# Performance work log

Hardware: AMD Instinct MI355X
Metric: run time of the kernel (lower is better)

The kernel has to match this reference:

```python
import jax, jax.numpy as jnp
import numpy as np

B, L, H, V = 256, 200, 128, 50000
NLAYER, K = 2, 20
NEG = -1e10


def setup_inputs() -> dict:
    key = jax.random.key(0)
    ks = jax.random.split(key, 14)
    lens = jax.random.randint(ks[0], (B,), 50, L + 1)
    pos = jnp.arange(L)
    valid = pos[None, :] < lens[:, None]                       # [B,L] bool
    seq = jnp.where(valid, jax.random.randint(ks[1], (B, L), 1, V), 0)
    lengths = valid.astype(jnp.int32)                          # >0 where real token
    reverse_lengths = jnp.where(valid, lens[:, None] - pos[None, :], 0)  # 1..len, 0=pad

    def nrm(k, shape, s=0.02):
        return jax.random.normal(k, shape, jnp.float32) * s

    emb_w = nrm(ks[2], (V, H)).at[0].set(0.0)
    wnoise_w = nrm(ks[3], (L + 1, H)).at[0].set(0.0)
    cluster_w = nrm(ks[4], (L + 1, 1)).at[0].set(0.0)
    ffn1_w = nrm(ks[5], (H, H), 0.05)
    ffn1_b = jnp.zeros((H,), jnp.float32)
    ffn2_w = nrm(ks[6], (H, H), 0.05)
    ffn2_b = jnp.zeros((H,), jnp.float32)
    ln_g = jnp.ones((H,), jnp.float32)
    ln_b = jnp.zeros((H,), jnp.float32)
    gate_w = nrm(ks[7], (2 * H, H), 0.05)
    coff = jax.random.normal(ks[8], (NLAYER, B, L, L), jnp.float32)  # fixed noise (torch.normal)
    return dict(seq=seq, lengths=lengths, reverse_lengths=reverse_lengths,
                emb_w=emb_w, wnoise_w=wnoise_w, cluster_w=cluster_w,
                ffn1_w=ffn1_w, ffn1_b=ffn1_b, ffn2_w=ffn2_w, ffn2_b=ffn2_b,
                ln_g=ln_g, ln_b=ln_b, gate_w=gate_w, coff=coff)


def _sp(x):  # torch.nn.Softplus(threshold=1): identity above 1
    return jnp.where(x > 1.0, x, jnp.log1p(jnp.exp(jnp.minimum(x, 1.0))))


def _forward(seq, lengths, reverse_lengths, emb_w, wnoise_w, cluster_w,
             ffn1_w, ffn1_b, ffn2_w, ffn2_b, ln_g, ln_b, gate_w, coff):
    b, l = seq.shape
    mask = (lengths > 0).astype(jnp.float32)                   # [B,L]
    hidden = emb_w[seq]                                        # [B,L,H]
    slen = jnp.sum(mask, axis=1)                               # [B]
    e_s = hidden[jnp.arange(b), (slen - 1).astype(jnp.int32)]  # last real token state
    zero_layer = jnp.sum(hidden, 1) / slen[:, None]
    layer_collect = [zero_layer]
    eye = jnp.eye(l, dtype=hidden.dtype)
    pair_ok = mask[:, :, None] * mask[:, None, :]              # [B,L,L]
    for i in range(coff.shape[0]):
        wn = wnoise_w[reverse_lengths]                         # [B,L,H]
        sim = jnp.einsum('bld,bmd->blm', hidden, hidden)
        nrm = jnp.linalg.norm(hidden, axis=2, keepdims=True)   # [B,L,1]
        sim = sim / (nrm * nrm.transpose(0, 2, 1) + 1e-6)      # cosine similarity
        diag = cluster_w[reverse_lengths][..., 0]              # [B,L]
        sim = sim + diag[:, :, None] * eye                     # diag_embed add
        sim = sim + coff[i] * _sp(jnp.einsum('bld,bmd->blm', hidden, wn))
        msim = jnp.where(pair_ok == 0.0, NEG, sim)             # masked_fill
        _, idx = jax.lax.top_k(msim, K)                        # [B,L,K]
        sel = jnp.zeros_like(msim).at[jnp.arange(b)[:, None, None],
                                      jnp.arange(l)[None, :, None], idx].set(1.0)
        edges = sel * (msim > NEG).astype(msim.dtype)          # top-k & above-threshold
        cluster_label = edges.transpose(0, 2, 1)
        sim_softmax = jax.nn.softmax(msim, axis=2)
        ssm = cluster_label * sim_softmax                      # [B,L,L] sparse-weighted
        update_hidden = jnp.einsum('blm,bmd->bld', ssm, hidden)
        cmask = jnp.sum(ssm, axis=2)                           # [B,L]
        cmask = cmask / jnp.maximum(jnp.linalg.norm(cmask, axis=1, keepdims=True), 1e-12)
        if i > 0:
            update_hidden = update_hidden * (slen > 1.0).astype(hidden.dtype)[:, None, None]
        feed1 = jax.nn.relu(update_hidden @ ffn1_w + ffn1_b)
        pre = feed1 @ ffn2_w + ffn2_b + update_hidden          # dropout = identity (eval)
        mu = jnp.mean(pre, -1, keepdims=True)
        var = jnp.var(pre, -1, keepdims=True)
        feed2 = (pre - mu) / jnp.sqrt(var + 1e-5) * ln_g + ln_b
        layer_collect.append(jnp.sum(feed2 * cmask[:, :, None], 1))
    e_c = jnp.mean(jnp.stack(layer_collect, 1), 1)             # [B,H]
    alpha = jax.nn.sigmoid(jnp.concatenate([e_c, e_s], -1) @ gate_w)
    sess = alpha * e_c + (1.0 - alpha) * e_s
    scores = sess @ emb_w.T                                    # [B,V]
    return scores


def reference(seq, lengths, reverse_lengths, emb_w, wnoise_w, cluster_w,
              ffn1_w, ffn1_b, ffn2_w, ffn2_b, ln_g, ln_b, gate_w, coff):
    scores = _forward(seq, lengths, reverse_lengths, emb_w, wnoise_w, cluster_w,
                      ffn1_w, ffn1_b, ffn2_w, ffn2_b, ln_g, ln_b, gate_w, coff)
    return (scores, jnp.asarray(0.0, jnp.float32))  # con_loss == 0 when abs=True
```

## Files before the change

### kernel.cpp

```cpp
#include <hip/hip_runtime.h>
#include <cstdint>
#include <cstddef>

namespace {
constexpr int B = 256, L = 200, H = 128, V = 50000, TK = 20;
constexpr int NT = 1563;
constexpr float NEGV = -1e10f;
}

using bf16x8 = __attribute__((ext_vector_type(8))) short;
using s16x8  = __attribute__((ext_vector_type(8))) short;
using f32x16 = __attribute__((ext_vector_type(16))) float;

__device__ inline unsigned short f2bf(float f) {
  unsigned int u = __float_as_uint(f);
  unsigned int r = (u + 0x7fffu + ((u >> 16) & 1u)) >> 16;
  return (unsigned short)r;
}

#define DPP_QUAD_XOR1 0xB1
#define DPP_QUAD_XOR2 0x4E
#define DPP_ROW_HMIRR 0x141
#define DPP_ROW_MIRR  0x140

template <int CTRL>
__device__ inline unsigned dpp16_max_step(unsigned v) {
  unsigned t = (unsigned)__builtin_amdgcn_update_dpp(0, (int)v, CTRL, 0xF, 0xF, true);
  return v > t ? v : t;
}
__device__ inline unsigned grp16_max(unsigned v) {
  v = dpp16_max_step<DPP_QUAD_XOR1>(v);
  v = dpp16_max_step<DPP_QUAD_XOR2>(v);
  v = dpp16_max_step<DPP_ROW_HMIRR>(v);
  v = dpp16_max_step<DPP_ROW_MIRR>(v);
  return v;
}
template <int CTRL>
__device__ inline float dpp16_add_step(float v) {
  int t = __builtin_amdgcn_update_dpp(0, __float_as_int(v), CTRL, 0xF, 0xF, true);
  return v + __int_as_float(t);
}
__device__ inline float grp16_sum(float v) {
  v = dpp16_add_step<DPP_QUAD_XOR1>(v);
  v = dpp16_add_step<DPP_QUAD_XOR2>(v);
  v = dpp16_add_step<DPP_ROW_HMIRR>(v);
  v = dpp16_add_step<DPP_ROW_MIRR>(v);
  return v;
}

__device__ inline unsigned f2key(float f) {
  unsigned b = __float_as_uint(f);
  unsigned m = (unsigned)((int)b >> 31);
  return b ^ (m | 0x80000000u);
}
__device__ inline float key2f(unsigned u) {
  unsigned b = (u & 0x80000000u) ? (u & 0x7fffffffu) : ~u;
  return __uint_as_float(b);
}

__global__ __launch_bounds__(256) void k_embed(const int* __restrict__ seq,
                                               const int* __restrict__ rev,
                                               const float* __restrict__ emb,
                                               const float* __restrict__ wnoise,
                                               float* __restrict__ hidden,
                                               float* __restrict__ nrm,
                                               s16x8* __restrict__ hbh,
                                               s16x8* __restrict__ hbl,
                                               s16x8* __restrict__ wnh,
                                               s16x8* __restrict__ wnl) {
  int b = blockIdx.x / 7, lt = blockIdx.x % 7;
  int t = threadIdx.x;
  int r = t >> 3, c2 = t & 7;
  int l = lt * 32 + r;
  bool valid = l < L;
  float vv[16], wv[16];
  if (valid) {
    int row = b * L + l;
    int tok = seq[row];
    const float4* ep = (const float4*)&emb[(size_t)tok * H + c2 * 16];
    const float4* wp = (const float4*)&wnoise[(size_t)rev[row] * H + c2 * 16];
#pragma unroll
    for (int i = 0; i < 4; ++i) {
      float4 x = ep[i];
      vv[i * 4 + 0] = x.x; vv[i * 4 + 1] = x.y; vv[i * 4 + 2] = x.z; vv[i * 4 + 3] = x.w;
      float4 y = wp[i];
      wv[i * 4 + 0] = y.x; wv[i * 4 + 1] = y.y; wv[i * 4 + 2] = y.z; wv[i * 4 + 3] = y.w;
    }
  } else {
#pragma unroll
    for (int i = 0; i < 16; ++i) { vv[i] = 0.f; wv[i] = 0.f; }
  }
  if (valid) {
    int row = b * L + l;
#pragma unroll
    for (int i = 0; i < 4; ++i)
      *(float4*)&hidden[(size_t)row * H + c2 * 16 + i * 4] =
          make_float4(vv[i * 4], vv[i * 4 + 1], vv[i * 4 + 2], vv[i * 4 + 3]);
    float s = 0.f;
#pragma unroll
    for (int i = 0; i < 16; ++i) s += vv[i] * vv[i];
    s += __shfl_down(s, 4, 8);
    s += __shfl_down(s, 2, 8);
    s += __shfl_down(s, 1, 8);
    if (c2 == 0) nrm[row] = sqrtf(s);
  }
  s16x8 h0, h1, l0, l1, w0, w1, x0, x1;
#pragma unroll
  for (int i = 0; i < 8; ++i) {
    unsigned short hi = f2bf(vv[i]);
    h0[i] = (short)hi;
    l0[i] = (short)f2bf(vv[i] - __uint_as_float((unsigned)hi << 16));
    unsigned short wh = f2bf(wv[i]);
    w0[i] = (short)wh;
    x0[i] = (short)f2bf(wv[i] - __uint_as_float((unsigned)wh << 16));
  }
#pragma unroll
  for (int i = 0; i < 8; ++i) {
    unsigned short hi = f2bf(vv[8 + i]);
    h1[i] = (short)hi;
    l1[i] = (short)f2bf(vv[8 + i] - __uint_as_float((unsigned)hi << 16));
    unsigned short wh = f2bf(wv[8 + i]);
    w1[i] = (short)wh;
    x1[i] = (short)f2bf(wv[8 + i] - __uint_as_float((unsigned)wh << 16));
  }
  size_t fi0 = ((size_t)(b * 7 + lt) * 8 + c2) * 64 + r;
  size_t fi1 = fi0 + 32;
  hbh[fi0] = h0; hbh[fi1] = h1;
  hbl[fi0] = l0; hbl[fi1] = l1;
  wnh[fi0] = w0; wnh[fi1] = w1;
  wnl[fi0] = x0; wnl[fi1] = x1;
}

__global__ __launch_bounds__(512) void k_init(const int* __restrict__ lengths,
                                              const float* __restrict__ hidden,
                                              float* __restrict__ ecacc,
                                              float* __restrict__ e_s) {
  int b = blockIdx.x, tid = threadIdx.x;
  __shared__ float part[4][128];
  __shared__ int wcnt[8];
  __shared__ int s_slen;
  int c = (tid < L && lengths[b * L + tid] > 0) ? 1 : 0;
  for (int o = 32; o > 0; o >>= 1) c += __shfl_down(c, o, 64);
  if ((tid & 63) == 0) wcnt[tid >> 6] = c;
  __syncthreads();
  if (tid == 0) {
    int s = 0;
#pragma unroll
    for (int i = 0; i < 8; ++i) s += wcnt[i];
    s_slen = s;
  }
  int h = tid & 127, seg = tid >> 7;
  float s = 0.f;
  for (int l = seg; l < L; l += 4) s += hidden[(size_t)(b * L + l) * H + h];
  part[seg][h] = s;
  __syncthreads();
  if (tid < 128) {
    float tot = part[0][h] + part[1][h] + part[2][h] + part[3][h];
    int slen = s_slen;
    ecacc[b * H + h] = tot / (float)slen;
    e_s[b * H + h] = hidden[(size_t)(b * L + slen - 1) * H + h];
  }
}

__global__ __launch_bounds__(256) void k_simws(const s16x8* __restrict__ hbh,
                                               const s16x8* __restrict__ hbl,
                                               const s16x8* __restrict__ wnh,
                                               const s16x8* __restrict__ wnl,
                                               const float* __restrict__ nrm,
                                               const int* __restrict__ rev,
                                               const float* __restrict__ cluster,
                                               float* __restrict__ S0,
                                               float* __restrict__ WS) {
  int orig = blockIdx.x;
  int xcd = orig & 7, slot = orig >> 3;
  int b = xcd * 32 + slot / 14;
  int rem = slot % 14;
  int lt = rem >> 1, half = rem & 1;
  int wid = threadIdx.x >> 6, lane = threadIdx.x & 63;
  int mt = half * 4 + wid;
  if (mt > 6) return;
  int lr = lane & 31, kh = lane >> 5;
  size_t abase = ((size_t)(b * 7 + lt) * 8) * 64 + lane;
  bf16x8 ah[8], al[8];
#pragma unroll
  for (int ks = 0; ks < 8; ++ks) {
    ah[ks] = (bf16x8)hbh[abase + ks * 64];
    al[ks] = (bf16x8)hbl[abase + ks * 64];
  }
  size_t bbase = ((size_t)(b * 7 + mt) * 8) * 64 + lane;
  f32x16 accs = {}, accw = {};
#pragma unroll
  for (int ks = 0; ks < 8; ++ks) {
    bf16x8 bhh = (bf16x8)hbh[bbase + ks * 64];
    bf16x8 bhl = (bf16x8)hbl[bbase + ks * 64];
    bf16x8 bwh = (bf16x8)wnh[bbase + ks * 64];
    bf16x8 bwl = (bf16x8)wnl[bbase + ks * 64];
    accs = __builtin_amdgcn_mfma_f32_32x32x16_bf16(ah[ks], bhh, accs, 0, 0, 0);
    accs = __builtin_amdgcn_mfma_f32_32x32x16_bf16(ah[ks], bhl, accs, 0, 0, 0);
    accs = __builtin_amdgcn_mfma_f32_32x32x16_bf16(al[ks], bhh, accs, 0, 0, 0);
    accw = __builtin_amdgcn_mfma_f32_32x32x16_bf16(ah[ks], bwh, accw, 0, 0, 0);
    accw = __builtin_amdgcn_mfma_f32_32x32x16_bf16(ah[ks], bwl, accw, 0, 0, 0);
    accw = __builtin_amdgcn_mfma_f32_32x32x16_bf16(al[ks], bwh, accw, 0, 0, 0);
  }
  int m = mt * 32 + lr;
  if (m < L) {
    float nm = nrm[b * L + m];
#pragma unroll
    for (int r = 0; r < 16; ++r) {
      int row = lt * 32 + (r & 3) + 8 * (r >> 2) + 4 * kh;
      if (row < L) {
        float nl = nrm[b * L + row];
        float s0 = accs[r] * __builtin_amdgcn_rcpf(nl * nm + 1e-6f);
        if (row == m) s0 += cluster[rev[b * L + row]];
        size_t o = (size_t)(b * L + row) * L + m;
        S0[o] = s0;
        float x = accw[r];
        WS[o] = (x > 1.f) ? x : __logf(1.f + __expf(x));
      }
    }
  }
}

__global__ __launch_bounds__(256) void k_rowpass(const float* __restrict__ S0,
                                                 const float* __restrict__ WS,
                                                 const float* __restrict__ coff_i,
                                                 const int* __restrict__ lengths,
                                                 float* __restrict__ P,
                                                 unsigned char* __restrict__ ET) {
  __shared__ unsigned klds[256 * 27];
  int wid = threadIdx.x >> 6, lane = threadIdx.x & 63;
  int g = lane >> 4, q = lane & 15;
  int bb = blockIdx.x / 7, blk = blockIdx.x % 7;
  int g16 = wid * 4 + g;
  int lA = blk * 32 + g16 * 2, lB = lA + 1;
  bool lvA = lA < L, lvB = lB < L;
  int lrowA = bb * L + (lvA ? lA : 0);
  int lrowB = bb * L + (lvB ? lB : 0);
  bool mA = lvA && (lengths[lrowA] > 0);
  bool mB = lvB && (lengths[lrowB] > 0);
  size_t baseA = (size_t)lrowA * L, baseB = (size_t)lrowB * L;
  int kbA = threadIdx.x * 27, kbB = kbA + 13;
  float valA[13], valB[13]; unsigned vmA = 0, vmB = 0;
  unsigned a0 = 0, a1 = 0, a2 = 0; int aj0 = 0, aj1 = 0, aj2 = 0;
  unsigned c0 = 0, c1 = 0, c2 = 0; int cj0 = 0, cj1 = 0, cj2 = 0;
#pragma unroll
  for (int j = 0; j < 13; ++j) {
    int m = q + 16 * j;
    bool colOk = (m < L) && (lengths[bb * L + m] > 0);
    bool okA = mA && colOk, okB = mB && colOk;
    float vA = 0.f, vB = 0.f;
    if (okA) vA = S0[baseA + m] + coff_i[baseA + m] * WS[baseA + m];
    if (okB) vB = S0[baseB + m] + coff_i[baseB + m] * WS[baseB + m];
    valA[j] = vA; valB[j] = vB;
    unsigned kA = okA ? f2key(vA) : 0u;
    unsigned kB = okB ? f2key(vB) : 0u;
    vmA |= okA ? (1u << j) : 0u;
    vmB |= okB ? (1u << j) : 0u;
    klds[kbA + j] = kA;
    klds[kbB + j] = kB;
    if (kA > a0)      { a2 = a1; aj2 = aj1; a1 = a0; aj1 = aj0; a0 = kA; aj0 = j; }
    else if (kA > a1) { a2 = a1; aj2 = aj1; a1 = kA; aj1 = j; }
    else if (kA > a2) { a2 = kA; aj2 = j; }
    if (kB > c0)      { c2 = c1; cj2 = cj1; c1 = c0; cj1 = cj0; c0 = kB; cj0 = j; }
    else if (kB > c1) { c2 = c1; cj2 = cj1; c1 = kB; cj1 = j; }
    else if (kB > c2) { c2 = kB; cj2 = j; }
  }
  unsigned ccA = a0; int cjA = aj0; int consA = 0;
  unsigned ccB = c0; int cjB = cj0; int consB = 0;
  unsigned MuA = 0u, MuB = 0u;
  for (int t = 0; t < TK; ++t) {
    unsigned gmA = grp16_max(ccA);
    unsigned gmB = grp16_max(ccB);
    if (t == 0) { MuA = gmA; MuB = gmB; }
    if (__all((gmA | gmB) == 0u)) break;
    unsigned long long balA = __ballot(ccA == gmA && gmA != 0u);
    unsigned long long balB = __ballot(ccB == gmB && gmB != 0u);
    unsigned long long grpm = 0xFFFFull << (g * 16);
    unsigned long long mineA = balA & grpm;
    unsigned long long mineB = balB & grpm;
    int ownA = mineA ? (int)__builtin_ctzll(mineA) : -1;
    int ownB = mineB ? (int)__builtin_ctzll(mineB) : -1;
    if (lane == ownA) {
      int m = q + 16 * cjA;
      ET[((size_t)bb * L + m) * L + lA] = 1;
      klds[kbA + cjA] = 0u;
      ++consA;
      if (consA == 1)      { ccA = a1; cjA = aj1; }
      else if (consA == 2) { ccA = a2; cjA = aj2; }
      else {
        unsigned x = 0; int xj = 0;
#pragma unroll
        for (int j = 0; j < 13; ++j) {
          unsigned k2 = klds[kbA + j];
          if (k2 > x) { x = k2; xj = j; }
        }
        ccA = x; cjA = xj;
      }
    }
    if (lane == ownB) {
      int m = q + 16 * cjB;
      ET[((size_t)bb * L + m) * L + lB] = 1;
      klds[kbB + cjB] = 0u;
      ++consB;
      if (consB == 1)      { ccB = c1; cjB = cj1; }
      else if (consB == 2) { ccB = c2; cjB = cj2; }
      else {
        unsigned x = 0; int xj = 0;
#pragma unroll
        for (int j = 0; j < 13; ++j) {
          unsigned k2 = klds[kbB + j];
          if (k2 > x) { x = k2; xj = j; }
        }
        ccB = x; cjB = xj;
      }
    }
  }
  float MA = key2f(MuA), MB = key2f(MuB);
  float eA[13], eB[13]; float sA = 0.f, sB = 0.f;
#pragma unroll
  for (int j = 0; j < 13; ++j) {
    float evA = ((vmA >> j) & 1u) ? __expf(valA[j] - MA) : 0.f;
    float evB = ((vmB >> j) & 1u) ? __expf(valB[j] - MB) : 0.f;
    eA[j] = evA; sA += evA;
    eB[j] = evB; sB += evB;
  }
  sA = grp16_sum(sA);
  sB = grp16_sum(sB);
  float invA = (sA > 0.f) ? __builtin_amdgcn_rcpf(sA) : 0.f;
  float invB = (sB > 0.f) ? __builtin_amdgcn_rcpf(sB) : 0.f;
#pragma unroll
  for (int j = 0; j < 13; ++j) {
    int m = q + 16 * j;
    if (m < L) {
      if (lvA) P[baseA + m] = eA[j] * invA;
      if (lvB) P[baseB + m] = eB[j] * invB;
    }
  }
}

__global__ __launch_bounds__(512) void k_gather(const float* __restrict__ P,
                                                const unsigned char* __restrict__ ET,
                                                const float* __restrict__ hidden,
                                                float* __restrict__ cmask,
                                                float* __restrict__ upd) {
  __shared__ float wls[4][224];
  __shared__ unsigned char ils[4][224];
  __shared__ int s_cnt[4];
  int wv = threadIdx.x >> 6, lane = threadIdx.x & 63;
  if (wv < 4) {
    int rowW = blockIdx.x * 4 + wv;
    size_t baseW = (size_t)rowW * L;
    float w[4]; float s = 0.f;
#pragma unroll
    for (int j = 0; j < 4; ++j) {
      int m = lane + 64 * j;
      float ww = 0.f;
      if (m < L) ww = P[baseW + m] * (float)ET[baseW + m];
      w[j] = ww; s += ww;
    }
    float ssum = s;
    for (int off = 1; off < 64; off <<= 1) ssum += __shfl_xor(ssum, off, 64);
    if (lane == 0) cmask[rowW] = ssum;
    int pos_base = 0;
#pragma unroll
    for (int j = 0; j < 4; ++j) {
      bool nz = (w[j] != 0.f);
      unsigned long long mk = __ballot(nz);
      int rank = __popcll(mk & ((1ull << lane) - 1ull));
      if (nz) {
        int pos = pos_base + rank;
        ils[wv][pos] = (unsigned char)(lane + 64 * j);
        wls[wv][pos] = w[j];
      }
      pos_base += (int)__popcll(mk);
    }
    if (lane == 0) s_cnt[wv] = pos_base;
    int padEnd = ((pos_base + TK - 1) / TK) * TK;
    for (int p = pos_base + lane; p < padEnd; p += 64) {
      ils[wv][p] = 0; wls[wv][p] = 0.f;
    }
  }
  __syncthreads();
  int half = threadIdx.x >> 7;
  int h = threadIdx.x & 127;
  int row = blockIdx.x * 4 + half;
  int b = row / L;
  int n = s_cnt[half];
  float acc = 0.f;
  for (int e0 = 0; e0 < n; e0 += TK) {
    float w[TK]; int m[TK];
#pragma unroll
    for (int e = 0; e < TK; ++e) { w[e] = wls[half][e0 + e]; m[e] = ils[half][e0 + e]; }
    float hv[TK];
#pragma unroll
    for (int e = 0; e < TK; ++e)
      hv[e] = hidden[(size_t)(b * L + m[e]) * H + h];
#pragma unroll
    for (int e = 0; e < TK; ++e)
      acc += w[e] * hv[e];
  }
  upd[(size_t)row * H + h] = acc;
}

__global__ __launch_bounds__(64) void k_cnorm(float* __restrict__ cmask) {
  int b = blockIdx.x, lane = threadIdx.x;
  float v[4]; float s = 0.f;
#pragma unroll
  for (int j = 0; j < 4; ++j) {
    int l = lane + 64 * j;
    float x = (l < L) ? cmask[b * L + l] : 0.f;
    v[j] = x; s += x * x;
  }
  for (int off = 1; off < 64; off <<= 1) s += __shfl_xor(s, off, 64);
  float inv = 1.f / fmaxf(sqrtf(s), 1e-12f);
#pragma unroll
  for (int j = 0; j < 4; ++j) {
    int l = lane + 64 * j;
    if (l < L) cmask[b * L + l] = v[j] * inv;
  }
}

__global__ __launch_bounds__(256) void k_ffn(float* __restrict__ upd,
                                             const float* __restrict__ W1,
                                             const float* __restrict__ b1,
                                             const float* __restrict__ W2,
                                             const float* __restrict__ b2,
                                             const float* __restrict__ g,
                                             const float* __restrict__ beta,
                                             const float* __restrict__ cmask) {
  constexpr int AS = 136;
  __shared__ __align__(16) char smem[4 * 64 * AS * 2];
  short* ahs = (short*)smem;
  short* als = ahs + 64 * AS;
  short* f1h = (short*)(smem + 2 * 64 * AS * 2);
  short* f1l = f1h + 64 * AS;
  float (*ps)[132] = (float (*)[132])smem;
  __shared__ float mus[64], rsd[64];
  int row0 = blockIdx.x * 64;
  int tid = threadIdx.x;
  int wid = tid >> 6, lane = tid & 63;
  int lr = lane & 31, kh = lane >> 5;
  int n0 = wid * 32;
  int n = n0 + lr;
#pragma unroll
  for (int it = 0; it < 8; ++it) {
    int f = it * 256 + tid;
    int r = f >> 5, c4 = (f & 31) * 4;
    float4 v = *(const float4*)&upd[(size_t)(row0 + r) * H + c4];
    float vv[4] = {v.x, v.y, v.z, v.w};
    unsigned short hh[4]; short ll[4];
#pragma unroll
    for (int q2 = 0; q2 < 4; ++q2) {
      hh[q2] = f2bf(vv[q2]);
      ll[q2] = (short)f2bf(vv[q2] - __uint_as_float((unsigned)hh[q2] << 16));
    }
    uint2 ph = make_uint2((unsigned)hh[0] | ((unsigned)hh[1] << 16),
                          (unsigned)hh[2] | ((unsigned)hh[3] << 16));
    uint2 pl = make_uint2((unsigned short)ll[0] | ((unsigned)(unsigned short)ll[1] << 16),
                          (unsigned short)ll[2] | ((unsigned)(unsigned short)ll[3] << 16));
    *(uint2*)&ahs[r * AS + c4] = ph;
    *(uint2*)&als[r * AS + c4] = pl;
  }
  __syncthreads();
  bf16x8 wfh[8], wfl[8];
#pragma unroll
  for (int ks = 0; ks < 8; ++ks) {
#pragma unroll
    for (int i = 0; i < 8; ++i) {
      float w = W1[(size_t)(ks * 16 + kh * 8 + i) * H + n];
      unsigned short hi = f2bf(w);
      wfh[ks][i] = (short)hi;
      wfl[ks][i] = (short)f2bf(w - __uint_as_float((unsigned)hi << 16));
    }
  }
  f32x16 acc0, acc1;
  {
    float bv = b1[n];
#pragma unroll
    for (int r = 0; r < 16; ++r) { acc0[r] = bv; acc1[r] = bv; }
  }
#pragma unroll
  for (int ks = 0; ks < 8; ++ks) {
    bf16x8 xh0 = *(const bf16x8*)&ahs[(0 * 32 + lr) * AS + ks * 16 + kh * 8];
    bf16x8 xl0 = *(const bf16x8*)&als[(0 * 32 + lr) * AS + ks * 16 + kh * 8];
    bf16x8 xh1 = *(const bf16x8*)&ahs[(1 * 32 + lr) * AS + ks * 16 + kh * 8];
    bf16x8 xl1 = *(const bf16x8*)&als[(1 * 32 + lr) * AS + ks * 16 + kh * 8];
    acc0 = __builtin_amdgcn_mfma_f32_32x32x16_bf16(xh0, wfh[ks], acc0, 0, 0, 0);
    acc0 = __builtin_amdgcn_mfma_f32_32x32x16_bf16(xl0, wfh[ks], acc0, 0, 0, 0);
    acc0 = __builtin_amdgcn_mfma_f32_32x32x16_bf16(xh0, wfl[ks], acc0, 0, 0, 0);
    acc1 = __builtin_amdgcn_mfma_f32_32x32x16_bf16(xh1, wfh[ks], acc1, 0, 0, 0);
    acc1 = __builtin_amdgcn_mfma_f32_32x32x16_bf16(xl1, wfh[ks], acc1, 0, 0, 0);
    acc1 = __builtin_amdgcn_mfma_f32_32x32x16_bf16(xh1, wfl[ks], acc1, 0, 0, 0);
  }
#pragma unroll
  for (int r = 0; r < 16; ++r) {
    int crow = (r & 3) + 8 * (r >> 2) + 4 * kh;
    float f0 = fmaxf(acc0[r], 0.f);
    unsigned short h0 = f2bf(f0);
    f1h[crow * AS + n] = (short)h0;
    f1l[crow * AS + n] = (short)f2bf(f0 - __uint_as_float((unsigned)h0 << 16));
    float f1v = fmaxf(acc1[r], 0.f);
    unsigned short h1 = f2bf(f1v);
    f1h[(32 + crow) * AS + n] = (short)h1;
    f1l[(32 + crow) * AS + n] = (short)f2bf(f1v - __uint_as_float((unsigned)h1 << 16));
  }
  __syncthreads();
#pragma unroll
  for (int ks = 0; ks < 8; ++ks) {
#pragma unroll
    for (int i = 0; i < 8; ++i) {
      float w = W2[(size_t)(ks * 16 + kh * 8 + i) * H + n];
      unsigned short hi = f2bf(w);
      wfh[ks][i] = (short)hi;
      wfl[ks][i] = (short)f2bf(w - __uint_as_float((unsigned)hi << 16));
    }
  }
  {
    float bv = b2[n];
#pragma unroll
    for (int r = 0; r < 16; ++r) { acc0[r] = bv; acc1[r] = bv; }
  }
#pragma unroll
  for (int ks = 0; ks < 8; ++ks) {
    bf16x8 xh0 = *(const bf16x8*)&f1h[(0 * 32 + lr) * AS + ks * 16 + kh * 8];
    bf16x8 xl0 = *(const bf16x8*)&f1l[(0 * 32 + lr) * AS + ks * 16 + kh * 8];
    bf16x8 xh1 = *(const bf16x8*)&f1h[(1 * 32 + lr) * AS + ks * 16 + kh * 8];
    bf16x8 xl1 = *(const bf16x8*)&f1l[(1 * 32 + lr) * AS + ks * 16 + kh * 8];
    acc0 = __builtin_amdgcn_mfma_f32_32x32x16_bf16(xh0, wfh[ks], acc0, 0, 0, 0);
    acc0 = __builtin_amdgcn_mfma_f32_32x32x16_bf16(xl0, wfh[ks], acc0, 0, 0, 0);
    acc0 = __builtin_amdgcn_mfma_f32_32x32x16_bf16(xh0, wfl[ks], acc0, 0, 0, 0);
    acc1 = __builtin_amdgcn_mfma_f32_32x32x16_bf16(xh1, wfh[ks], acc1, 0, 0, 0);
    acc1 = __builtin_amdgcn_mfma_f32_32x32x16_bf16(xl1, wfh[ks], acc1, 0, 0, 0);
    acc1 = __builtin_amdgcn_mfma_f32_32x32x16_bf16(xh1, wfl[ks], acc1, 0, 0, 0);
  }
#pragma unroll
  for (int r = 0; r < 16; ++r) {
    int crow = (r & 3) + 8 * (r >> 2) + 4 * kh;
    float p0 = acc0[r] + upd[(size_t)(row0 + crow) * H + n];
    float p1 = acc1[r] + upd[(size_t)(row0 + 32 + crow) * H + n];
    acc0[r] = p0; acc1[r] = p1;
    ps[crow][n] = p0;
    ps[32 + crow][n] = p1;
  }
  __syncthreads();
  {
    int r = tid >> 2, sub = tid & 3;
    float s = 0.f, sq = 0.f;
#pragma unroll
    for (int j = 0; j < 8; ++j) {
      float4 x = *(const float4*)&ps[r][sub * 32 + j * 4];
      s += x.x + x.y + x.z + x.w;
      sq += x.x * x.x + x.y * x.y + x.z * x.z + x.w * x.w;
    }
    s += __shfl_down(s, 2, 4);  s += __shfl_down(s, 1, 4);
    sq += __shfl_down(sq, 2, 4); sq += __shfl_down(sq, 1, 4);
    if (sub == 0) {
      float mu = s * (1.f / 128.f);
      float var = sq * (1.f / 128.f) - mu * mu;
      mus[r] = mu;
      rsd[r] = rsqrtf(var + 1e-5f);
    }
  }
  __syncthreads();
  {
    float gn = g[n], bn = beta[n];
#pragma unroll
    for (int r = 0; r < 16; ++r) {
      int crow = (r & 3) + 8 * (r >> 2) + 4 * kh;
      float o0 = ((acc0[r] - mus[crow]) * rsd[crow] * gn + bn) * cmask[row0 + crow];
      float o1 = ((acc1[r] - mus[32 + crow]) * rsd[32 + crow] * gn + bn) * cmask[row0 + 32 + crow];
      upd[(size_t)(row0 + crow) * H + n] = o0;
      upd[(size_t)(row0 + 32 + crow) * H + n] = o1;
    }
  }
}

__global__ __launch_bounds__(512) void k_ecadd(const float* __restrict__ wf,
                                               float* __restrict__ ecacc) {
  int b = blockIdx.x, tid = threadIdx.x;
  __shared__ float part[4][128];
  int h = tid & 127, seg = tid >> 7;
  float s = 0.f;
  for (int l = seg; l < L; l += 4) s += wf[(size_t)(b * L + l) * H + h];
  part[seg][h] = s;
  __syncthreads();
  if (tid < 128)
    ecacc[b * H + h] += part[0][h] + part[1][h] + part[2][h] + part[3][h];
}

__global__ __launch_bounds__(256) void k_embconv(const float* __restrict__ emb,
                                                 s16x8* __restrict__ ebh,
                                                 s16x8* __restrict__ ebl) {
  int nt = blockIdx.x;
  int t = threadIdx.x;
  int r = t >> 3, c2 = t & 7;
  int n = nt * 32 + r;
  float vv[16];
  if (n < V) {
    const float4* ep = (const float4*)&emb[(size_t)n * H + c2 * 16];
#pragma unroll
    for (int i = 0; i < 4; ++i) {
      float4 x = ep[i];
      vv[i * 4 + 0] = x.x; vv[i * 4 + 1] = x.y; vv[i * 4 + 2] = x.z; vv[i * 4 + 3] = x.w;
    }
  } else {
#pragma unroll
    for (int i = 0; i < 16; ++i) vv[i] = 0.f;
  }
  s16x8 h0, h1, l0, l1;
#pragma unroll
  for (int i = 0; i < 8; ++i) {
    unsigned short hi = f2bf(vv[i]);
    h0[i] = (short)hi;
    l0[i] = (short)f2bf(vv[i] - __uint_as_float((unsigned)hi << 16));
    unsigned short hj = f2bf(vv[8 + i]);
    h1[i] = (short)hj;
    l1[i] = (short)f2bf(vv[8 + i] - __uint_as_float((unsigned)hj << 16));
  }
  size_t fi0 = ((size_t)nt * 8 + c2) * 64 + r;
  size_t fi1 = fi0 + 32;
  ebh[fi0] = h0; ebh[fi1] = h1;
  ebl[fi0] = l0; ebl[fi1] = l1;
}

__global__ __launch_bounds__(128) void k_gate(const float* __restrict__ ecacc,
                                              const float* __restrict__ e_s,
                                              const float* __restrict__ gw,
                                              float* __restrict__ sess,
                                              float* __restrict__ out) {
  __shared__ float cat[256];
  int b = blockIdx.x, h = threadIdx.x;
  float ec = ecacc[b * H + h] * (1.f / 3.f);
  float es = e_s[b * H + h];
  cat[h] = ec; cat[128 + h] = es;
  __syncthreads();
  float a = 0.f;
  for (int j = 0; j < 256; ++j) a = fmaf(cat[j], gw[(size_t)j * H + h], a);
  a = 1.f / (1.f + __expf(-a));
  sess[b * H + h] = a * ec + (1.f - a) * es;
  if (b == 0 && h == 0) out[(size_t)B * V] = 0.f;
}

__global__ __launch_bounds__(256) void k_scores(const float* __restrict__ sess,
                                                const s16x8* __restrict__ ebh,
                                                const s16x8* __restrict__ ebl,
                                                float* __restrict__ out) {
  int wid = threadIdx.x >> 6, lane = threadIdx.x & 63;
  int lr = lane & 31, kh = lane >> 5;
  int mt = blockIdx.y;
  int m = mt * 32 + lr;
  bf16x8 ah[8], al[8];
#pragma unroll
  for (int ks = 0; ks < 8; ++ks) {
    const float* sp = &sess[(size_t)m * H + ks * 16 + kh * 8];
    float4 a = *(const float4*)sp;
    float4 c = *(const float4*)(sp + 4);
    float av[8] = {a.x, a.y, a.z, a.w, c.x, c.y, c.z, c.w};
#pragma unroll
    for (int i = 0; i < 8; ++i) {
      unsigned short hi = f2bf(av[i]);
      ah[ks][i] = (short)hi;
      al[ks][i] = (short)f2bf(av[i] - __uint_as_float((unsigned)hi << 16));
    }
  }
  int ntEnd = min(blockIdx.x * 16 + 16, NT);
  for (int nt = blockIdx.x * 16 + wid; nt < ntEnd; nt += 4) {
    size_t bbase = ((size_t)nt * 8) * 64 + lane;
    f32x16 acc = {};
#pragma unroll
    for (int ks = 0; ks < 8; ++ks) {
      bf16x8 bh = (bf16x8)ebh[bbase + ks * 64];
      bf16x8 bl = (bf16x8)ebl[bbase + ks * 64];
      acc = __builtin_amdgcn_mfma_f32_32x32x16_bf16(ah[ks], bh, acc, 0, 0, 0);
      acc = __builtin_amdgcn_mfma_f32_32x32x16_bf16(al[ks], bh, acc, 0, 0, 0);
      acc = __builtin_amdgcn_mfma_f32_32x32x16_bf16(ah[ks], bl, acc, 0, 0, 0);
    }
    int n = nt * 32 + lr;
    if (n < V) {
#pragma unroll
      for (int r = 0; r < 16; ++r) {
        int row = mt * 32 + (r & 3) + 8 * (r >> 2) + 4 * kh;
        out[(size_t)row * V + n] = acc[r];
      }
    }
  }
}

extern "C" void kernel_launch(void* const* d_in, const int* in_sizes, int n_in,
                              void* d_out, int out_size, void* d_ws, size_t ws_size,
                              hipStream_t stream) {
  const int*   seq  = (const int*)d_in[0];
  const int*   lens = (const int*)d_in[1];
  const int*   rev  = (const int*)d_in[2];
  const float* emb  = (const float*)d_in[3];
  const float* wnz  = (const float*)d_in[4];
  const float* clw  = (const float*)d_in[5];
  const float* w1   = (const float*)d_in[6];
  const float* fb1  = (const float*)d_in[7];
  const float* w2   = (const float*)d_in[8];
  const float* fb2  = (const float*)d_in[9];
  const float* lng  = (const float*)d_in[10];
  const float* lnb  = (const float*)d_in[11];
  const float* gw   = (const float*)d_in[12];
  const float* coff = (const float*)d_in[13];
  float* out = (float*)d_out;

  char* ws = (char*)d_ws;
  size_t off = 0;
  auto alloc = [&](size_t bytes) {
    void* p = ws + off;
    off += (bytes + 255) & ~(size_t)255;
    return p;
  };
  float* hidden = (float*)alloc((size_t)B * L * H * 4);
  float* nrm    = (float*)alloc((size_t)B * L * 4);
  float* S0     = (float*)alloc((size_t)B * L * L * 4);
  float* WS     = (float*)alloc((size_t)B * L * L * 4);
  float* P      = (float*)alloc((size_t)B * L * L * 4);
  float* upd    = (float*)alloc((size_t)B * L * H * 4);
  float* cmask  = (float*)alloc((size_t)B * L * 4);
  int*   cnt    = (int*)alloc((size_t)B * L * 4);
  float* e_s    = (float*)alloc((size_t)B * H * 4);
  float* ecacc  = (float*)alloc((size_t)B * H * 4);
  float* sess   = (float*)alloc((size_t)B * H * 4);
  unsigned char* ET = (unsigned char*)alloc((size_t)B * L * L);
  s16x8* hbh = (s16x8*)alloc((size_t)B * 7 * 8 * 64 * 16);
  s16x8* wnh = (s16x8*)alloc((size_t)B * 7 * 8 * 64 * 16);
  s16x8* hbl = (s16x8*)P;
  s16x8* wnl = (s16x8*)upd;
  s16x8* ebh = (s16x8*)S0;
  s16x8* ebl = (s16x8*)WS;

  k_embed<<<B * 7, 256, 0, stream>>>(seq, rev, emb, wnz, hidden, nrm,
                                     hbh, hbl, wnh, wnl);
  k_init<<<B, 512, 0, stream>>>(lens, hidden, ecacc, e_s);
  k_simws<<<B * 14, 256, 0, stream>>>(hbh, hbl, wnh, wnl, nrm, rev, clw, S0, WS);

  for (int i = 0; i < 2; ++i) {
    hipMemsetAsync(ET, 0, (size_t)B * L * L, stream);
    k_rowpass<<<B * 7, 256, 0, stream>>>(S0, WS, coff + (size_t)i * B * L * L,
                                         lens, P, ET);
    k_gather<<<B * L / 4, 512, 0, stream>>>(P, ET, hidden, cmask, upd);
    k_cnorm<<<B, 64, 0, stream>>>(cmask);
    k_ffn<<<B * L / 64, 256, 0, stream>>>(upd, w1, fb1, w2, fb2, lng, lnb, cmask);
    k_ecadd<<<B, 512, 0, stream>>>(upd, ecacc);
  }

  k_embconv<<<NT, 256, 0, stream>>>(emb, ebh, ebl);
  k_gate<<<B, 128, 0, stream>>>(ecacc, e_s, gw, sess, out);
  k_scores<<<dim3((NT + 15) / 16, 8), 256, 0, stream>>>(sess, ebh, ebl, out);
}
```

Measured before the change: 463.4 us.

## Compute both layers' row-pass in one kernel sharing S0/WS loads

The per-layer row-pass kernel is replaced by a single kernel that handles both layers, because S0 and WS do not depend on the layer. Each row's S0/WS values are read once and combined with both layers' noise tensors, producing two probability matrices and two top-k edge masks. The LDS key buffer is dropped in favour of a consumed-bitmask that recomputes keys from registers. The cost is an extra full P buffer and ET buffer, plus higher register pressure from holding two layers' state per thread.

```diff
diff --git a/kernel.cpp b/kernel.cpp
--- a/kernel.cpp
+++ b/kernel.cpp
@@ -221,52 +221,52 @@
   }
 }
 
-__global__ __launch_bounds__(256) void k_rowpass(const float* __restrict__ S0,
-                                                 const float* __restrict__ WS,
-                                                 const float* __restrict__ coff_i,
-                                                 const int* __restrict__ lengths,
-                                                 float* __restrict__ P,
-                                                 unsigned char* __restrict__ ET) {
-  __shared__ unsigned klds[256 * 27];
+__global__ __launch_bounds__(256) void k_rowpass2(const float* __restrict__ S0,
+                                                  const float* __restrict__ WS,
+                                                  const float* __restrict__ coff,
+                                                  const int* __restrict__ lengths,
+                                                  float* __restrict__ P1,
+                                                  float* __restrict__ P2,
+                                                  unsigned char* __restrict__ ET1,
+                                                  unsigned char* __restrict__ ET2) {
   int wid = threadIdx.x >> 6, lane = threadIdx.x & 63;
   int g = lane >> 4, q = lane & 15;
-  int bb = blockIdx.x / 7, blk = blockIdx.x % 7;
-  int g16 = wid * 4 + g;
-  int lA = blk * 32 + g16 * 2, lB = lA + 1;
-  bool lvA = lA < L, lvB = lB < L;
-  int lrowA = bb * L + (lvA ? lA : 0);
-  int lrowB = bb * L + (lvB ? lB : 0);
-  bool mA = lvA && (lengths[lrowA] > 0);
-  bool mB = lvB && (lengths[lrowB] > 0);
-  size_t baseA = (size_t)lrowA * L, baseB = (size_t)lrowB * L;
-  int kbA = threadIdx.x * 27, kbB = kbA + 13;
-  float valA[13], valB[13]; unsigned vmA = 0, vmB = 0;
+  int bb = blockIdx.x / 13, blk = blockIdx.x % 13;
+  int l = blk * 16 + wid * 4 + g;
+  bool lvalid = l < L;
+  int lrow = bb * L + (lvalid ? l : 0);
+  bool mask_l = lvalid && (lengths[lrow] > 0);
+  size_t base = (size_t)lrow * L;
+  const float* c0 = coff;
+  const float* c1 = coff + (size_t)B * L * L;
+  float valA[13], valB[13]; unsigned okm = 0;
   unsigned a0 = 0, a1 = 0, a2 = 0; int aj0 = 0, aj1 = 0, aj2 = 0;
-  unsigned c0 = 0, c1 = 0, c2 = 0; int cj0 = 0, cj1 = 0, cj2 = 0;
+  unsigned b0 = 0, b1 = 0, b2 = 0; int bj0 = 0, bj1 = 0, bj2 = 0;
 #pragma unroll
   for (int j = 0; j < 13; ++j) {
     int m = q + 16 * j;
-    bool colOk = (m < L) && (lengths[bb * L + m] > 0);
-    bool okA = mA && colOk, okB = mB && colOk;
-    float vA = 0.f, vB = 0.f;
-    if (okA) vA = S0[baseA + m] + coff_i[baseA + m] * WS[baseA + m];
-    if (okB) vB = S0[baseB + m] + coff_i[baseB + m] * WS[baseB + m];
+    bool ok = false; float vA = 0.f, vB = 0.f;
+    if (mask_l && m < L) {
+      ok = lengths[bb * L + m] > 0;
+      if (ok) {
+        float a = S0[base + m], w = WS[base + m];
+        vA = a + c0[base + m] * w;
+        vB = a + c1[base + m] * w;
+      }
+    }
     valA[j] = vA; valB[j] = vB;
-    unsigned kA = okA ? f2key(vA) : 0u;
-    unsigned kB = okB ? f2key(vB) : 0u;
-    vmA |= okA ? (1u << j) : 0u;
-    vmB |= okB ? (1u << j) : 0u;
-    klds[kbA + j] = kA;
-    klds[kbB + j] = kB;
+    okm |= ok ? (1u << j) : 0u;
+    unsigned kA = ok ? f2key(vA) : 0u;
+    unsigned kB = ok ? f2key(vB) : 0u;
     if (kA > a0)      { a2 = a1; aj2 = aj1; a1 = a0; aj1 = aj0; a0 = kA; aj0 = j; }
     else if (kA > a1) { a2 = a1; aj2 = aj1; a1 = kA; aj1 = j; }
     else if (kA > a2) { a2 = kA; aj2 = j; }
-    if (kB > c0)      { c2 = c1; cj2 = cj1; c1 = c0; cj1 = cj0; c0 = kB; cj0 = j; }
-    else if (kB > c1) { c2 = c1; cj2 = cj1; c1 = kB; cj1 = j; }
-    else if (kB > c2) { c2 = kB; cj2 = j; }
-  }
-  unsigned ccA = a0; int cjA = aj0; int consA = 0;
-  unsigned ccB = c0; int cjB = cj0; int consB = 0;
+    if (kB > b0)      { b2 = b1; bj2 = bj1; b1 = b0; bj1 = bj0; b0 = kB; bj0 = j; }
+    else if (kB > b1) { b2 = b1; bj2 = bj1; b1 = kB; bj1 = j; }
+    else if (kB > b2) { b2 = kB; bj2 = j; }
+  }
+  unsigned ccA = a0; int cjA = aj0; int consA = 0; unsigned cmA = 0;
+  unsigned ccB = b0; int cjB = bj0; int consB = 0; unsigned cmB = 0;
   unsigned MuA = 0u, MuB = 0u;
   for (int t = 0; t < TK; ++t) {
     unsigned gmA = grp16_max(ccA);
@@ -282,8 +282,8 @@
     int ownB = mineB ? (int)__builtin_ctzll(mineB) : -1;
     if (lane == ownA) {
       int m = q + 16 * cjA;
-      ET[((size_t)bb * L + m) * L + lA] = 1;
-      klds[kbA + cjA] = 0u;
+      ET1[((size_t)bb * L + m) * L + l] = 1;
+      cmA |= 1u << cjA;
       ++consA;
       if (consA == 1)      { ccA = a1; cjA = aj1; }
       else if (consA == 2) { ccA = a2; cjA = aj2; }
@@ -291,7 +291,8 @@
         unsigned x = 0; int xj = 0;
 #pragma unroll
         for (int j = 0; j < 13; ++j) {
-          unsigned k2 = klds[kbA + j];
+          bool avail = ((okm >> j) & 1u) && !((cmA >> j) & 1u);
+          unsigned k2 = avail ? f2key(valA[j]) : 0u;
           if (k2 > x) { x = k2; xj = j; }
         }
         ccA = x; cjA = xj;
@@ -299,16 +300,17 @@
     }
     if (lane == ownB) {
       int m = q + 16 * cjB;
-      ET[((size_t)bb * L + m) * L + lB] = 1;
-      klds[kbB + cjB] = 0u;
+      ET2[((size_t)bb * L + m) * L + l] = 1;
+      cmB |= 1u << cjB;
       ++consB;
-      if (consB == 1)      { ccB = c1; cjB = cj1; }
-      else if (consB == 2) { ccB = c2; cjB = cj2; }
+      if (consB == 1)      { ccB = b1; cjB = bj1; }
+      else if (consB == 2) { ccB = b2; cjB = bj2; }
       else {
         unsigned x = 0; int xj = 0;
 #pragma unroll
         for (int j = 0; j < 13; ++j) {
-          unsigned k2 = klds[kbB + j];
+          bool avail = ((okm >> j) & 1u) && !((cmB >> j) & 1u);
+          unsigned k2 = avail ? f2key(valB[j]) : 0u;
           if (k2 > x) { x = k2; xj = j; }
         }
         ccB = x; cjB = xj;
@@ -319,8 +321,9 @@
   float eA[13], eB[13]; float sA = 0.f, sB = 0.f;
 #pragma unroll
   for (int j = 0; j < 13; ++j) {
-    float evA = ((vmA >> j) & 1u) ? __expf(valA[j] - MA) : 0.f;
-    float evB = ((vmB >> j) & 1u) ? __expf(valB[j] - MB) : 0.f;
+    bool ok = (okm >> j) & 1u;
+    float evA = ok ? __expf(valA[j] - MA) : 0.f;
+    float evB = ok ? __expf(valB[j] - MB) : 0.f;
     eA[j] = evA; sA += evA;
     eB[j] = evB; sB += evB;
   }
@@ -328,12 +331,14 @@
   sB = grp16_sum(sB);
   float invA = (sA > 0.f) ? __builtin_amdgcn_rcpf(sA) : 0.f;
   float invB = (sB > 0.f) ? __builtin_amdgcn_rcpf(sB) : 0.f;
-#pragma unroll
-  for (int j = 0; j < 13; ++j) {
-    int m = q + 16 * j;
-    if (m < L) {
-      if (lvA) P[baseA + m] = eA[j] * invA;
-      if (lvB) P[baseB + m] = eB[j] * invB;
+  if (lvalid) {
+#pragma unroll
+    for (int j = 0; j < 13; ++j) {
+      int m = q + 16 * j;
+      if (m < L) {
+        P1[base + m] = eA[j] * invA;
+        P2[base + m] = eB[j] * invB;
+      }
     }
   }
 }
@@ -716,17 +721,18 @@
   float* nrm    = (float*)alloc((size_t)B * L * 4);
   float* S0     = (float*)alloc((size_t)B * L * L * 4);
   float* WS     = (float*)alloc((size_t)B * L * L * 4);
-  float* P      = (float*)alloc((size_t)B * L * L * 4);
+  float* P1     = (float*)alloc((size_t)B * L * L * 4);
+  float* P2     = (float*)alloc((size_t)B * L * L * 4);
   float* upd    = (float*)alloc((size_t)B * L * H * 4);
   float* cmask  = (float*)alloc((size_t)B * L * 4);
-  int*   cnt    = (int*)alloc((size_t)B * L * 4);
   float* e_s    = (float*)alloc((size_t)B * H * 4);
   float* ecacc  = (float*)alloc((size_t)B * H * 4);
   float* sess   = (float*)alloc((size_t)B * H * 4);
-  unsigned char* ET = (unsigned char*)alloc((size_t)B * L * L);
+  unsigned char* ET1 = (unsigned char*)alloc((size_t)B * L * L);
+  unsigned char* ET2 = (unsigned char*)alloc((size_t)B * L * L);
   s16x8* hbh = (s16x8*)alloc((size_t)B * 7 * 8 * 64 * 16);
   s16x8* wnh = (s16x8*)alloc((size_t)B * 7 * 8 * 64 * 16);
-  s16x8* hbl = (s16x8*)P;
+  s16x8* hbl = (s16x8*)P1;
   s16x8* wnl = (s16x8*)upd;
   s16x8* ebh = (s16x8*)S0;
   s16x8* ebl = (s16x8*)WS;
@@ -736,10 +742,13 @@
   k_init<<<B, 512, 0, stream>>>(lens, hidden, ecacc, e_s);
   k_simws<<<B * 14, 256, 0, stream>>>(hbh, hbl, wnh, wnl, nrm, rev, clw, S0, WS);
 
+  hipMemsetAsync(ET1, 0, (size_t)B * L * L, stream);
+  hipMemsetAsync(ET2, 0, (size_t)B * L * L, stream);
+  k_rowpass2<<<B * 13, 256, 0, stream>>>(S0, WS, coff, lens, P1, P2, ET1, ET2);
+
   for (int i = 0; i < 2; ++i) {
-    hipMemsetAsync(ET, 0, (size_t)B * L * L, stream);
-    k_rowpass<<<B * 7, 256, 0, stream>>>(S0, WS, coff + (size_t)i * B * L * L,
-                                         lens, P, ET);
+    float* P = i ? P2 : P1;
+    unsigned char* ET = i ? ET2 : ET1;
     k_gather<<<B * L / 4, 512, 0, stream>>>(P, ET, hidden, cmask, upd);
     k_cnorm<<<B, 64, 0, stream>>>(cmask);
     k_ffn<<<B * L / 64, 256, 0, stream>>>(upd, w1, fb1, w2, fb2, lng, lnb, cmask);
```

After: 448.1 us. 3.3% less time.
